# Kernel tuning notes

Hardware: AMD Instinct MI355X
Metric: run time of the kernel (lower is better)

The kernel has to match this reference:

```python
import jax, jax.numpy as jnp
import numpy as np

N = 1024
IN_CH = 128
EDGE_CH = 32
OUT_CH = 128


def setup_inputs() -> dict:
    key = jax.random.key(0)
    ks = jax.random.split(key, 8)
    return {
        "node_mat": jax.random.normal(ks[0], (N, IN_CH), dtype=jnp.float32),
        "adj": jax.random.uniform(ks[1], (N, N), dtype=jnp.float32),
        "edge_adj": jax.random.uniform(ks[2], (EDGE_CH, N, N), dtype=jnp.float32),
        "node_weight": jax.random.normal(ks[3], (IN_CH, OUT_CH), dtype=jnp.float32) * 0.05,
        "edge_lay_1": jax.random.normal(ks[4], (EDGE_CH, OUT_CH - 1), dtype=jnp.float32) * 0.05,
        "edge_lay_2": jax.random.normal(ks[5], (OUT_CH - 1, OUT_CH), dtype=jnp.float32) * 0.05,
        "root": jax.random.normal(ks[6], (IN_CH, OUT_CH), dtype=jnp.float32) * 0.05,
        "bias": jax.random.normal(ks[7], (OUT_CH,), dtype=jnp.float32) * 0.05,
    }


def reference(node_mat, adj, edge_adj, node_weight, edge_lay_1, edge_lay_2, root, bias):
    # node message passing: adj-weighted sum of transformed node features  [N, out]
    sum_filter_node_msgs = adj @ (node_mat @ node_weight)
    # edge MLP: 2-layer with ReLU, applied over the edge-channel axis
    # edge_adj: [E, N, N]; edge_lay_1: [E, out-1] -> h1: [out-1, N, N]
    h1 = jnp.maximum(jnp.einsum('enm,eb->bnm', edge_adj, edge_lay_1), 0.0)
    # h1: [out-1, N, N]; edge_lay_2: [out-1, out] -> h2: [out, N, N]
    h2 = jnp.einsum('bnm,bo->onm', h1, edge_lay_2)
    # adjacency-weighted compression: e_compress[n, o] = sum_m h2[o, n, m] * adj[n, m]
    e_compress = jnp.einsum('onm,nm->no', h2, adj)
    root_info = node_mat @ root
    return sum_filter_node_msgs + e_compress + root_info + bias
```

## Files before the change

kernel.cpp:

```cpp
#include <hip/hip_runtime.h>
#include <hip/hip_bf16.h>

#define NN 1024
#define IN_CH 128
#define EDGE_CH 32
#define OUT_CH 128
#define NNSQ ((size_t)NN * (size_t)NN)

typedef __attribute__((ext_vector_type(8))) short bf16x8;
typedef __attribute__((ext_vector_type(4))) float f32x4;

static __device__ __forceinline__ short f2bf(float f) {
    union { float f; unsigned u; } v; v.f = f;
    unsigned r = v.u + 0x7FFFu + ((v.u >> 16) & 1u);
    return (short)(r >> 16);
}

__global__ void node_gemm_kernel(const float* __restrict__ node_mat,
                                 const float* __restrict__ node_weight,
                                 const float* __restrict__ root,
                                 short* __restrict__ PT,
                                 float* __restrict__ R) {
    __shared__ float nm[2 * IN_CH];
    int tid = threadIdx.x;
    int n0 = blockIdx.x * 2;
    nm[tid] = node_mat[n0 * IN_CH + tid];
    __syncthreads();
    int o = tid & 127;
    int h = tid >> 7;
    const float* nr = &nm[h * IN_CH];
    float accp = 0.f, accr = 0.f;
#pragma unroll 8
    for (int c = 0; c < IN_CH; ++c) {
        float x = nr[c];
        accp += x * node_weight[c * OUT_CH + o];
        accr += x * root[c * OUT_CH + o];
    }
    R[(size_t)(n0 + h) * OUT_CH + o] = accr;
    PT[(size_t)o * NN + (n0 + h)] = f2bf(accp);
}

__global__ void adjp_kernel(const float* __restrict__ adj,
                            const short* __restrict__ PT,
                            const float* __restrict__ R,
                            const float* __restrict__ bias,
                            float* __restrict__ out) {
    int blk = blockIdx.x;
    int nb = blk & 63;
    int oh = blk >> 6;
    int tid = threadIdx.x;
    int wave = tid >> 6;
    int lane = tid & 63;
    int quad = lane >> 4;
    int col  = lane & 15;
    int n0 = nb * 16;
    int o0 = oh * 64;

    f32x4 acc[4];
#pragma unroll
    for (int ot = 0; ot < 4; ++ot) acc[ot] = (f32x4){0.f, 0.f, 0.f, 0.f};

    int kbase = wave * 256;
#pragma unroll
    for (int ks = 0; ks < 8; ++ks) {
        int k = kbase + ks * 32 + quad * 8;
        const float* ap = adj + (size_t)(n0 + col) * NN + k;
        f32x4 a0 = *(const f32x4*)ap;
        f32x4 a1 = *(const f32x4*)(ap + 4);
        bf16x8 a;
#pragma unroll
        for (int j = 0; j < 4; ++j) { a[j] = f2bf(a0[j]); a[4 + j] = f2bf(a1[j]); }
#pragma unroll
        for (int ot = 0; ot < 4; ++ot) {
            int o = o0 + ot * 16 + col;
            bf16x8 b = *(const bf16x8*)(PT + (size_t)o * NN + k);
            acc[ot] = __builtin_amdgcn_mfma_f32_16x16x32_bf16(a, b, acc[ot], 0, 0, 0);
        }
    }

    __shared__ float red[4][16][65];
#pragma unroll
    for (int ot = 0; ot < 4; ++ot)
#pragma unroll
        for (int r = 0; r < 4; ++r)
            red[wave][quad * 4 + r][ot * 16 + col] = acc[ot][r];
    __syncthreads();

#pragma unroll
    for (int i = tid; i < 16 * 64; i += 256) {
        int rr = i >> 6;
        int cc = i & 63;
        float v = red[0][rr][cc] + red[1][rr][cc] + red[2][rr][cc] + red[3][rr][cc];
        size_t idx = (size_t)(n0 + rr) * OUT_CH + o0 + cc;
        out[idx] = v + R[idx] + bias[o0 + cc];
    }
}

__global__ void __launch_bounds__(256, 3)
edge_out_kernel(const float* __restrict__ edge_adj,
                const float* __restrict__ adj,
                const float* __restrict__ L1,
                const float* __restrict__ L2,
                float* __restrict__ out) {
    int n = blockIdx.x;
    int tid = threadIdx.x;
    int wave = tid >> 6;
    int lane = tid & 63;
    int quad = lane >> 4;
    int col  = lane & 15;

    __shared__ __attribute__((aligned(16))) short ea_lds[2][256 * 40];
    __shared__ float adj_lds[NN];
    __shared__ float gs[OUT_CH];
    __shared__ float part[2][OUT_CH];

    *(f32x4*)&adj_lds[tid * 4] = *(const f32x4*)(adj + (size_t)n * NN + tid * 4);

    bf16x8 a_frag0, a_frag1;
#pragma unroll
    for (int j = 0; j < 8; ++j) {
        int e = quad * 8 + j;
        int b0 = (wave * 2 + 0) * 16 + col;
        int b1 = (wave * 2 + 1) * 16 + col;
        a_frag0[j] = f2bf((b0 < OUT_CH - 1) ? L1[e * (OUT_CH - 1) + b0] : 0.0f);
        a_frag1[j] = f2bf((b1 < OUT_CH - 1) ? L1[e * (OUT_CH - 1) + b1] : 0.0f);
    }

    float g0[4] = {0.f, 0.f, 0.f, 0.f};
    float g1[4] = {0.f, 0.f, 0.f, 0.f};

    const float* ea_b = edge_adj + (size_t)(wave * 8) * NNSQ + (size_t)n * NN + lane * 4;

    f32x4 stA0, stA1, stA2, stA3, stA4, stA5, stA6, stA7;
    f32x4 stB0, stB1, stB2, stB3, stB4, stB5, stB6, stB7;

#define NTLD(P) __builtin_nontemporal_load((const f32x4*)(P))
#define ISSUE_A(AC) { \
        const float* p_ = ea_b + (AC) * 256; \
        stA0 = NTLD(p_ + 0 * NNSQ); stA1 = NTLD(p_ + 1 * NNSQ); \
        stA2 = NTLD(p_ + 2 * NNSQ); stA3 = NTLD(p_ + 3 * NNSQ); \
        stA4 = NTLD(p_ + 4 * NNSQ); stA5 = NTLD(p_ + 5 * NNSQ); \
        stA6 = NTLD(p_ + 6 * NNSQ); stA7 = NTLD(p_ + 7 * NNSQ); }
#define ISSUE_B(AC) { \
        const float* p_ = ea_b + (AC) * 256; \
        stB0 = NTLD(p_ + 0 * NNSQ); stB1 = NTLD(p_ + 1 * NNSQ); \
        stB2 = NTLD(p_ + 2 * NNSQ); stB3 = NTLD(p_ + 3 * NNSQ); \
        stB4 = NTLD(p_ + 4 * NNSQ); stB5 = NTLD(p_ + 5 * NNSQ); \
        stB6 = NTLD(p_ + 6 * NNSQ); stB7 = NTLD(p_ + 7 * NNSQ); }
#define CONVERT_A(BUF) { \
        _Pragma("unroll") for (int k = 0; k < 4; ++k) { \
            bf16x8 pk_; \
            pk_[0] = f2bf(stA0[k]); pk_[1] = f2bf(stA1[k]); \
            pk_[2] = f2bf(stA2[k]); pk_[3] = f2bf(stA3[k]); \
            pk_[4] = f2bf(stA4[k]); pk_[5] = f2bf(stA5[k]); \
            pk_[6] = f2bf(stA6[k]); pk_[7] = f2bf(stA7[k]); \
            *(bf16x8*)((BUF) + (lane * 4 + k) * 40 + wave * 8) = pk_; } }
#define CONVERT_B(BUF) { \
        _Pragma("unroll") for (int k = 0; k < 4; ++k) { \
            bf16x8 pk_; \
            pk_[0] = f2bf(stB0[k]); pk_[1] = f2bf(stB1[k]); \
            pk_[2] = f2bf(stB2[k]); pk_[3] = f2bf(stB3[k]); \
            pk_[4] = f2bf(stB4[k]); pk_[5] = f2bf(stB5[k]); \
            pk_[6] = f2bf(stB6[k]); pk_[7] = f2bf(stB7[k]); \
            *(bf16x8*)((BUF) + (lane * 4 + k) * 40 + wave * 8) = pk_; } }
#define COMPUTE(BUF, AC) { \
        _Pragma("unroll") for (int st = 0; st < 16; ++st) { \
            int mrow = st * 16 + col; \
            float adjv = adj_lds[(AC) * 256 + mrow]; \
            bf16x8 bfv = *(const bf16x8*)((BUF) + mrow * 40 + quad * 8); \
            f32x4 d0 = __builtin_amdgcn_mfma_f32_16x16x32_bf16( \
                a_frag0, bfv, (f32x4){0.f, 0.f, 0.f, 0.f}, 0, 0, 0); \
            f32x4 d1 = __builtin_amdgcn_mfma_f32_16x16x32_bf16( \
                a_frag1, bfv, (f32x4){0.f, 0.f, 0.f, 0.f}, 0, 0, 0); \
            _Pragma("unroll") for (int r = 0; r < 4; ++r) { \
                g0[r] += fmaxf(d0[r], 0.0f) * adjv; \
                g1[r] += fmaxf(d1[r], 0.0f) * adjv; } } }

    const int c0 = n & 3, c1 = (n + 1) & 3, c2 = (n + 2) & 3, c3 = (n + 3) & 3;
    short* buf0 = &ea_lds[0][0];
    short* buf1 = &ea_lds[1][0];

    ISSUE_A(c0); ISSUE_B(c1);
    CONVERT_A(buf0);
    __syncthreads();

    ISSUE_A(c2);
    COMPUTE(buf0, c0);
    CONVERT_B(buf1);
    __syncthreads();

    ISSUE_B(c3);
    COMPUTE(buf1, c1);
    CONVERT_A(buf0);
    __syncthreads();

    COMPUTE(buf0, c2);
    CONVERT_B(buf1);
    __syncthreads();

    COMPUTE(buf1, c3);

#undef NTLD
#undef ISSUE_A
#undef ISSUE_B
#undef CONVERT_A
#undef CONVERT_B
#undef COMPUTE

#pragma unroll
    for (int r = 0; r < 4; ++r) {
        float v0 = g0[r], v1 = g1[r];
        v0 += __shfl_xor(v0, 1); v1 += __shfl_xor(v1, 1);
        v0 += __shfl_xor(v0, 2); v1 += __shfl_xor(v1, 2);
        v0 += __shfl_xor(v0, 4); v1 += __shfl_xor(v1, 4);
        v0 += __shfl_xor(v0, 8); v1 += __shfl_xor(v1, 8);
        g0[r] = v0; g1[r] = v1;
    }

    if (col == 0) {
#pragma unroll
        for (int r = 0; r < 4; ++r) {
            gs[(wave * 2 + 0) * 16 + quad * 4 + r] = g0[r];
            gs[(wave * 2 + 1) * 16 + quad * 4 + r] = g1[r];
        }
    }
    __syncthreads();

    int o = tid & 127;
    int hf = tid >> 7;
    float acc = 0.f;
    int blo = hf * 64, bhi = hf ? 127 : 64;
#pragma unroll 8
    for (int b = blo; b < bhi; ++b)
        acc += gs[b] * L2[b * OUT_CH + o];
    part[hf][o] = acc;
    __syncthreads();
    if (tid < 128) {
        size_t idx = (size_t)n * OUT_CH + tid;
        out[idx] += part[0][tid] + part[1][tid];
    }
}

extern "C" void kernel_launch(void* const* d_in, const int* in_sizes, int n_in,
                              void* d_out, int out_size, void* d_ws, size_t ws_size,
                              hipStream_t stream) {
    const float* node_mat    = (const float*)d_in[0];
    const float* adj         = (const float*)d_in[1];
    const float* edge_adj    = (const float*)d_in[2];
    const float* node_weight = (const float*)d_in[3];
    const float* edge_lay_1  = (const float*)d_in[4];
    const float* edge_lay_2  = (const float*)d_in[5];
    const float* root        = (const float*)d_in[6];
    const float* bias        = (const float*)d_in[7];
    float* out = (float*)d_out;

    short* PT = (short*)d_ws;
    float* R  = (float*)((char*)d_ws + OUT_CH * NN * sizeof(short));

    node_gemm_kernel<<<NN / 2, 256, 0, stream>>>(node_mat, node_weight, root, PT, R);
    adjp_kernel<<<128, 256, 0, stream>>>(adj, PT, R, bias, out);
    edge_out_kernel<<<NN, 256, 0, stream>>>(edge_adj, adj, edge_lay_1,
                                            edge_lay_2, out);
}
```

Measured before the change: 238.2 us.

## Split edge kernel rows across two blocks and combine with atomics

Each node row's m-range is split between two blocks, doubling the grid and halving per-block LDS and register staging (64-bit loads instead of 128-bit). Launch bounds raise the target occupancy to 6 blocks per CU to hide HBM latency better. Partial outputs are combined via atomicAdd into out, which adds atomic traffic, nondeterministic summation order, and possible register pressure from the tighter launch bound.

```diff
diff --git a/kernel.cpp b/kernel.cpp
--- a/kernel.cpp
+++ b/kernel.cpp
@@ -9,6 +9,7 @@
 
 typedef __attribute__((ext_vector_type(8))) short bf16x8;
 typedef __attribute__((ext_vector_type(4))) float f32x4;
+typedef __attribute__((ext_vector_type(2))) float f32x2;
 
 static __device__ __forceinline__ short f2bf(float f) {
     union { float f; unsigned u; } v; v.f = f;
@@ -96,25 +97,28 @@
     }
 }
 
-__global__ void __launch_bounds__(256, 3)
+__global__ void __launch_bounds__(256, 6)
 edge_out_kernel(const float* __restrict__ edge_adj,
                 const float* __restrict__ adj,
                 const float* __restrict__ L1,
                 const float* __restrict__ L2,
                 float* __restrict__ out) {
-    int n = blockIdx.x;
+    int n    = blockIdx.x >> 1;
+    int half = blockIdx.x & 1;
     int tid = threadIdx.x;
     int wave = tid >> 6;
     int lane = tid & 63;
     int quad = lane >> 4;
     int col  = lane & 15;
 
-    __shared__ __attribute__((aligned(16))) short ea_lds[2][256 * 40];
-    __shared__ float adj_lds[NN];
+    __shared__ __attribute__((aligned(16))) short ea_lds[2][128 * 40];
+    __shared__ float adj_lds[512];
     __shared__ float gs[OUT_CH];
     __shared__ float part[2][OUT_CH];
 
-    *(f32x4*)&adj_lds[tid * 4] = *(const f32x4*)(adj + (size_t)n * NN + tid * 4);
+    int mbase = half * 512;
+    if (tid < 128)
+        *(f32x4*)&adj_lds[tid * 4] = *(const f32x4*)(adj + (size_t)n * NN + mbase + tid * 4);
 
     bf16x8 a_frag0, a_frag1;
 #pragma unroll
@@ -129,44 +133,45 @@
     float g0[4] = {0.f, 0.f, 0.f, 0.f};
     float g1[4] = {0.f, 0.f, 0.f, 0.f};
 
-    const float* ea_b = edge_adj + (size_t)(wave * 8) * NNSQ + (size_t)n * NN + lane * 4;
-
-    f32x4 stA0, stA1, stA2, stA3, stA4, stA5, stA6, stA7;
-    f32x4 stB0, stB1, stB2, stB3, stB4, stB5, stB6, stB7;
-
-#define NTLD(P) __builtin_nontemporal_load((const f32x4*)(P))
+    const float* ea_b = edge_adj + (size_t)(wave * 8) * NNSQ + (size_t)n * NN
+                        + mbase + lane * 2;
+
+    f32x2 stA0, stA1, stA2, stA3, stA4, stA5, stA6, stA7;
+    f32x2 stB0, stB1, stB2, stB3, stB4, stB5, stB6, stB7;
+
+#define NTLD(P) __builtin_nontemporal_load((const f32x2*)(P))
 #define ISSUE_A(AC) { \
-        const float* p_ = ea_b + (AC) * 256; \
+        const float* p_ = ea_b + (AC) * 128; \
         stA0 = NTLD(p_ + 0 * NNSQ); stA1 = NTLD(p_ + 1 * NNSQ); \
         stA2 = NTLD(p_ + 2 * NNSQ); stA3 = NTLD(p_ + 3 * NNSQ); \
         stA4 = NTLD(p_ + 4 * NNSQ); stA5 = NTLD(p_ + 5 * NNSQ); \
         stA6 = NTLD(p_ + 6 * NNSQ); stA7 = NTLD(p_ + 7 * NNSQ); }
 #define ISSUE_B(AC) { \
-        const float* p_ = ea_b + (AC) * 256; \
+        const float* p_ = ea_b + (AC) * 128; \
         stB0 = NTLD(p_ + 0 * NNSQ); stB1 = NTLD(p_ + 1 * NNSQ); \
         stB2 = NTLD(p_ + 2 * NNSQ); stB3 = NTLD(p_ + 3 * NNSQ); \
         stB4 = NTLD(p_ + 4 * NNSQ); stB5 = NTLD(p_ + 5 * NNSQ); \
         stB6 = NTLD(p_ + 6 * NNSQ); stB7 = NTLD(p_ + 7 * NNSQ); }
 #define CONVERT_A(BUF) { \
-        _Pragma("unroll") for (int k = 0; k < 4; ++k) { \
+        _Pragma("unroll") for (int k = 0; k < 2; ++k) { \
             bf16x8 pk_; \
             pk_[0] = f2bf(stA0[k]); pk_[1] = f2bf(stA1[k]); \
             pk_[2] = f2bf(stA2[k]); pk_[3] = f2bf(stA3[k]); \
             pk_[4] = f2bf(stA4[k]); pk_[5] = f2bf(stA5[k]); \
             pk_[6] = f2bf(stA6[k]); pk_[7] = f2bf(stA7[k]); \
-            *(bf16x8*)((BUF) + (lane * 4 + k) * 40 + wave * 8) = pk_; } }
+            *(bf16x8*)((BUF) + (lane * 2 + k) * 40 + wave * 8) = pk_; } }
 #define CONVERT_B(BUF) { \
-        _Pragma("unroll") for (int k = 0; k < 4; ++k) { \
+        _Pragma("unroll") for (int k = 0; k < 2; ++k) { \
             bf16x8 pk_; \
             pk_[0] = f2bf(stB0[k]); pk_[1] = f2bf(stB1[k]); \
             pk_[2] = f2bf(stB2[k]); pk_[3] = f2bf(stB3[k]); \
             pk_[4] = f2bf(stB4[k]); pk_[5] = f2bf(stB5[k]); \
             pk_[6] = f2bf(stB6[k]); pk_[7] = f2bf(stB7[k]); \
-            *(bf16x8*)((BUF) + (lane * 4 + k) * 40 + wave * 8) = pk_; } }
+            *(bf16x8*)((BUF) + (lane * 2 + k) * 40 + wave * 8) = pk_; } }
 #define COMPUTE(BUF, AC) { \
-        _Pragma("unroll") for (int st = 0; st < 16; ++st) { \
+        _Pragma("unroll") for (int st = 0; st < 8; ++st) { \
             int mrow = st * 16 + col; \
-            float adjv = adj_lds[(AC) * 256 + mrow]; \
+            float adjv = adj_lds[(AC) * 128 + mrow]; \
             bf16x8 bfv = *(const bf16x8*)((BUF) + mrow * 40 + quad * 8); \
             f32x4 d0 = __builtin_amdgcn_mfma_f32_16x16x32_bf16( \
                 a_frag0, bfv, (f32x4){0.f, 0.f, 0.f, 0.f}, 0, 0, 0); \
@@ -176,7 +181,8 @@
                 g0[r] += fmaxf(d0[r], 0.0f) * adjv; \
                 g1[r] += fmaxf(d1[r], 0.0f) * adjv; } } }
 
-    const int c0 = n & 3, c1 = (n + 1) & 3, c2 = (n + 2) & 3, c3 = (n + 3) & 3;
+    const int base = (n + half) & 3;
+    const int c0 = base, c1 = (base + 1) & 3, c2 = (base + 2) & 3, c3 = (base + 3) & 3;
     short* buf0 = &ea_lds[0][0];
     short* buf1 = &ea_lds[1][0];
 
@@ -235,10 +241,8 @@
         acc += gs[b] * L2[b * OUT_CH + o];
     part[hf][o] = acc;
     __syncthreads();
-    if (tid < 128) {
-        size_t idx = (size_t)n * OUT_CH + tid;
-        out[idx] += part[0][tid] + part[1][tid];
-    }
+    if (tid < 128)
+        atomicAdd(&out[(size_t)n * OUT_CH + tid], part[0][tid] + part[1][tid]);
 }
 
 extern "C" void kernel_launch(void* const* d_in, const int* in_sizes, int n_in,
@@ -259,6 +263,6 @@
 
     node_gemm_kernel<<<NN / 2, 256, 0, stream>>>(node_mat, node_weight, root, PT, R);
     adjp_kernel<<<128, 256, 0, stream>>>(adj, PT, R, bias, out);
-    edge_out_kernel<<<NN, 256, 0, stream>>>(edge_adj, adj, edge_lay_1,
-                                            edge_lay_2, out);
-}
+    edge_out_kernel<<<2 * NN, 256, 0, stream>>>(edge_adj, adj, edge_lay_1,
+                                                edge_lay_2, out);
+}
```

Measured after the change: 310.0 us. 30.2% more time.
